# Kernel optimization log

Hardware: AMD Instinct MI355X
Metric: run time of the kernel (lower is better)

## Reference

```python
import jax, jax.numpy as jnp
import numpy as np
import math

HEADS = 4
DIM_HEAD = 32
EPS = 1e-5

def _ln_channels(x):
    # LayerNorm over channel axis (axis=1) of NCHW, no affine (eps=1e-5)
    mu = jnp.mean(x, axis=1, keepdims=True)
    var = jnp.mean((x - mu) ** 2, axis=1, keepdims=True)
    return (x - mu) * jax.lax.rsqrt(var + EPS)

def setup_inputs() -> dict:
    key = jax.random.key(0)
    k1, k2, k3, k4 = jax.random.split(key, 4)
    dim, inner = 256, HEADS * DIM_HEAD
    x = jax.random.normal(k1, (16, dim, 64, 64), dtype=jnp.float32)
    Wqkv = jax.random.normal(k2, (3 * inner, dim), dtype=jnp.float32) * (1.0 / math.sqrt(dim))
    Wout = jax.random.normal(k3, (dim, inner), dtype=jnp.float32) * (1.0 / math.sqrt(inner))
    bout = jax.random.normal(k4, (dim,), dtype=jnp.float32) * 0.01
    return {"x": x, "Wqkv": Wqkv, "Wout": Wout, "bout": bout}

def reference(x, Wqkv, Wout, bout):
    B, C, H, W = x.shape
    N = H * W
    inner = HEADS * DIM_HEAD
    # pre-norm (channel-wise LayerNorm via permute in torch)
    normed = _ln_channels(x)
    # 1x1 conv to qkv: [B, 3*inner, H, W]
    qkv = jnp.einsum('oc,bchw->bohw', Wqkv, normed)
    q, k, v = jnp.split(qkv, 3, axis=1)
    # [B, inner, H, W] -> [B, heads, N, dim_head]
    def to_heads(t):
        return t.reshape(B, HEADS, DIM_HEAD, N).transpose(0, 1, 3, 2)
    q, k, v = to_heads(q), to_heads(k), to_heads(v)
    q = jax.nn.softmax(q, axis=-1)          # over dim_head
    k = jax.nn.softmax(k, axis=-2)          # over N
    q = q / math.sqrt(DIM_HEAD)
    v = v / N
    context = jnp.einsum('bhnd,bhne->bhde', k, v)   # [B,h,d,d]
    out = jnp.einsum('bhde,bhnd->bhne', context, q) # [B,h,N,d]
    out = out.transpose(0, 1, 3, 2).reshape(B, inner, H, W)
    out = jnp.einsum('oc,bchw->bohw', Wout, out) + bout[None, :, None, None]
    out = _ln_channels(out)                  # LinearAttention.out_norm
    return out + x                           # residual
```

## Files before the change

### kernel.cpp

```cpp
#include <hip/hip_runtime.h>
#include <hip/hip_bf16.h>
#include <math.h>

#define BATCH 16
#define CH 256
#define NPOS 4096
#define INNER 128
#define HEADS 4
#define DH 32

typedef __hip_bfloat16 bf16;
typedef short bf8v __attribute__((ext_vector_type(8)));
typedef float f32x4 __attribute__((ext_vector_type(4)));

__device__ __forceinline__ float b2f(bf16 v) { return __bfloat162float(v); }
__device__ __forceinline__ float us2f(unsigned short u) {
    unsigned w = ((unsigned)u) << 16; float f; __builtin_memcpy(&f, &w, 4); return f;
}
__device__ __forceinline__ unsigned short f2us(float f) {
    bf16 h = __float2bfloat16(f); unsigned short u; __builtin_memcpy(&u, &h, 2); return u;
}
__device__ __forceinline__ bf16 f2b(float v) { return __float2bfloat16(v); }

__global__ __launch_bounds__(256)
void prep_w_kernel(const float* __restrict__ Wqkv, bf16* __restrict__ wqb,
                   float* __restrict__ wqs) {
    int idx = (blockIdx.x * 256 + threadIdx.x) * 4;
    float4 w = *(const float4*)&Wqkv[idx];
    ushort4 u;
    u.x = f2us(w.x); u.y = f2us(w.y); u.z = f2us(w.z); u.w = f2us(w.w);
    *(ushort4*)&wqb[idx] = u;
    float s4 = us2f(u.x) + us2f(u.y) + us2f(u.z) + us2f(u.w);
    #pragma unroll
    for (int m = 1; m <= 32; m <<= 1) s4 += __shfl_xor(s4, m, 64);
    if ((threadIdx.x & 63) == 0)
        wqs[blockIdx.x * 4 + (threadIdx.x >> 6)] = s4;
}

__global__ __launch_bounds__(256)
void fused_qkv_kernel(const float* __restrict__ x, const bf16* __restrict__ wqb,
                      const float* __restrict__ wqs,
                      bf16* __restrict__ p, float* __restrict__ ctxp) {
    __shared__ char smem[36864];
    __shared__ float stats[640];

    const int b = blockIdx.y, tile = blockIdx.x, n0 = tile * 64;
    const int tid = threadIdx.x;
    const int w = tid >> 6, lane = tid & 63;
    const int lrow = lane & 15, kq = lane >> 4;
    bf16* A = (bf16*)smem;

    {
        const int nq = tid & 15, cp = tid >> 4;
        float s[4] = {0.f,0.f,0.f,0.f}, sq[4] = {0.f,0.f,0.f,0.f};
        #pragma unroll
        for (int i = 0; i < 8; ++i) {
            int c0 = cp * 2 + 32 * i;
            const float* xp = x + ((size_t)b * CH + c0) * NPOS + n0 + nq * 4;
            float4 fa = *(const float4*)xp;
            float4 fb = *(const float4*)(xp + NPOS);
            #pragma unroll
            for (int j = 0; j < 4; ++j) {
                float va = (&fa.x)[j], vb = (&fb.x)[j];
                s[j] += va + vb; sq[j] += va * va + vb * vb;
                *(unsigned*)&A[(nq * 4 + j) * 264 + c0] =
                    (unsigned)f2us(va) | ((unsigned)f2us(vb) << 16);
            }
        }
        #pragma unroll
        for (int j = 0; j < 4; ++j) {
            s[j]  += __shfl_xor(s[j], 16, 64);  sq[j] += __shfl_xor(sq[j], 16, 64);
            s[j]  += __shfl_xor(s[j], 32, 64);  sq[j] += __shfl_xor(sq[j], 32, 64);
            if (lane < 16) {
                stats[(nq * 4 + j) * 8 + w * 2]     = s[j];
                stats[(nq * 4 + j) * 8 + w * 2 + 1] = sq[j];
            }
        }
    }
    __syncthreads();
    if (tid < 64) {
        float s  = stats[tid*8] + stats[tid*8+2] + stats[tid*8+4] + stats[tid*8+6];
        float sq = stats[tid*8+1] + stats[tid*8+3] + stats[tid*8+5] + stats[tid*8+7];
        float m = s * (1.f / 256.f);
        float var = sq * (1.f / 256.f) - m * m;
        stats[512 + tid * 2] = m;
        stats[512 + tid * 2 + 1] = rsqrtf(var + 1e-5f);
    }
    __syncthreads();

    ushort4 ekp[4][2];
    float se0 = 0.f, se1 = 0.f;

    for (int ph = 0; ph < 3; ++ph) {
        const bf16* wp = wqb + (size_t)(ph * 128 + w * 32) * 256;
        const float cs0 = wqs[ph * 128 + w * 32 + lrow];
        const float cs1 = wqs[ph * 128 + w * 32 + 16 + lrow];
        f32x4 acc[4][2];
        #pragma unroll
        for (int i = 0; i < 4; ++i) {
            acc[i][0] = (f32x4){0.f,0.f,0.f,0.f};
            acc[i][1] = (f32x4){0.f,0.f,0.f,0.f};
        }
        #pragma unroll 2
        for (int k0 = 0; k0 < 256; k0 += 32) {
            bf8v af[4], bfr[2];
            #pragma unroll
            for (int t = 0; t < 4; ++t)
                af[t] = *(const bf8v*)&A[(t * 16 + lrow) * 264 + k0 + kq * 8];
            #pragma unroll
            for (int t = 0; t < 2; ++t)
                bfr[t] = *(const bf8v*)&wp[(size_t)(t * 16 + lrow) * 256 + k0 + kq * 8];
            #pragma unroll
            for (int mt = 0; mt < 4; ++mt)
                #pragma unroll
                for (int nt = 0; nt < 2; ++nt)
                    acc[mt][nt] = __builtin_amdgcn_mfma_f32_16x16x32_bf16(
                        af[mt], bfr[nt], acc[mt][nt], 0, 0, 0);
        }

        if (ph == 0) {
            unsigned* pg32 = (unsigned*)p;
            #pragma unroll
            for (int mt = 0; mt < 4; ++mt)
                #pragma unroll
                for (int r = 0; r < 4; ++r) {
                    int row = mt * 16 + kq * 4 + r;
                    float mu = stats[512 + row * 2], rsn = stats[512 + row * 2 + 1];
                    float e0 = __expf(b2f(f2b((acc[mt][0][r] - mu * cs0) * rsn)));
                    float e1 = __expf(b2f(f2b((acc[mt][1][r] - mu * cs1) * rsn)));
                    float s = e0 + e1;
                    s += __shfl_xor(s, 1, 64);  s += __shfl_xor(s, 2, 64);
                    s += __shfl_xor(s, 4, 64);  s += __shfl_xor(s, 8, 64);
                    float rd = 1.f / s;
                    pg32[(size_t)(b * NPOS + n0 + row) * 64 + w * 16 + lrow] =
                        (unsigned)f2us(e0 * rd) | ((unsigned)f2us(e1 * rd) << 16);
                }
        } else if (ph == 1) {
            se0 = 0.f; se1 = 0.f;
            #pragma unroll
            for (int mt = 0; mt < 4; ++mt) {
                ushort4 u0, u1;
                unsigned short q_;
                #pragma unroll
                for (int r = 0; r < 4; ++r) {
                    int row = mt * 16 + kq * 4 + r;
                    float mu = stats[512 + row * 2], rsn = stats[512 + row * 2 + 1];
                    q_ = f2us(__expf(b2f(f2b((acc[mt][0][r] - mu * cs0) * rsn))));
                    se0 += us2f(q_); (&u0.x)[r] = q_;
                    q_ = f2us(__expf(b2f(f2b((acc[mt][1][r] - mu * cs1) * rsn))));
                    se1 += us2f(q_); (&u1.x)[r] = q_;
                }
                ekp[mt][0] = u0; ekp[mt][1] = u1;
            }
            se0 += __shfl_xor(se0, 16, 64); se0 += __shfl_xor(se0, 32, 64);
            se1 += __shfl_xor(se1, 16, 64); se1 += __shfl_xor(se1, 32, 64);
        } else {
            __syncthreads();
            bf16* ekt = (bf16*)(smem + w * 9216);
            bf16* vt  = (bf16*)(smem + w * 9216 + 4608);
            #pragma unroll
            for (int mt = 0; mt < 4; ++mt)
                #pragma unroll
                for (int nt = 0; nt < 2; ++nt) {
                    float csx = nt ? cs1 : cs0;
                    ushort4 vv;
                    #pragma unroll
                    for (int r = 0; r < 4; ++r) {
                        int row = mt * 16 + kq * 4 + r;
                        float mu = stats[512 + row * 2], rsn = stats[512 + row * 2 + 1];
                        (&vv.x)[r] = f2us((acc[mt][nt][r] - mu * csx) * rsn);
                    }
                    int d = nt * 16 + lrow, n = mt * 16 + kq * 4;
                    *(ushort4*)&vt[d * 72 + n]  = vv;
                    *(ushort4*)&ekt[d * 72 + n] = ekp[mt][nt];
                }
            f32x4 cacc[2][2];
            cacc[0][0] = (f32x4){0.f,0.f,0.f,0.f}; cacc[0][1] = cacc[0][0];
            cacc[1][0] = cacc[0][0];               cacc[1][1] = cacc[0][0];
            #pragma unroll
            for (int ks = 0; ks < 2; ++ks) {
                bf8v a2[2], bv2[2];
                a2[0]  = *(const bf8v*)&ekt[lrow * 72 + ks * 32 + kq * 8];
                a2[1]  = *(const bf8v*)&ekt[(16 + lrow) * 72 + ks * 32 + kq * 8];
                bv2[0] = *(const bf8v*)&vt[lrow * 72 + ks * 32 + kq * 8];
                bv2[1] = *(const bf8v*)&vt[(16 + lrow) * 72 + ks * 32 + kq * 8];
                #pragma unroll
                for (int mt2 = 0; mt2 < 2; ++mt2)
                    #pragma unroll
                    for (int nt2 = 0; nt2 < 2; ++nt2)
                        cacc[mt2][nt2] = __builtin_amdgcn_mfma_f32_16x16x32_bf16(
                            a2[mt2], bv2[nt2], cacc[mt2][nt2], 0, 0, 0);
            }
            float* pb = ctxp + ((size_t)(b * 64 + tile) * 4 + w) * 1056;
            #pragma unroll
            for (int mt2 = 0; mt2 < 2; ++mt2)
                #pragma unroll
                for (int nt2 = 0; nt2 < 2; ++nt2)
                    #pragma unroll
                    for (int r = 0; r < 4; ++r) {
                        int d = mt2 * 16 + kq * 4 + r, e = nt2 * 16 + lrow;
                        pb[d * 32 + e] = cacc[mt2][nt2][r];
                    }
            if (kq == 0) {
                pb[1024 + lrow] = se0;
                pb[1024 + 16 + lrow] = se1;
            }
        }
    }
}

__global__ __launch_bounds__(256)
void ctx_wmod_kernel(const float* __restrict__ ctxp, const float* __restrict__ Wout,
                     bf16* __restrict__ wmod) {
    __shared__ float cs[1056];
    int h = blockIdx.x, b = blockIdx.y, ch = blockIdx.z;
    int tid = threadIdx.x;

    #pragma unroll
    for (int i = 0; i < 2; ++i) {
        int s = i * 256 + tid;
        if (s < 264) {
            f32x4 a = (f32x4){0.f,0.f,0.f,0.f};
            const float* src = ctxp + (size_t)(b * 64 * 4 + h) * 1056 + s * 4;
            for (int t = 0; t < 64; ++t)
                a += *(const f32x4*)(src + (size_t)t * 4 * 1056);
            *(f32x4*)&cs[s * 4] = a;
        }
    }
    __syncthreads();

    int c = ch * 128 + (tid >> 1);
    int dh = tid & 1;
    const float* wr = Wout + (size_t)c * INNER + h * DH;
    float wv[32];
    #pragma unroll
    for (int i = 0; i < 8; ++i) {
        float4 t = *(const float4*)&wr[i * 4];
        wv[i * 4] = t.x; wv[i * 4 + 1] = t.y; wv[i * 4 + 2] = t.z; wv[i * 4 + 3] = t.w;
    }
    const float SCALE = 4.3158341e-05f;
    unsigned* wm32 = (unsigned*)(wmod + ((size_t)b * CH + c) * INNER + h * DH);
    #pragma unroll
    for (int dd = 0; dd < 8; ++dd) {
        int d1 = dh * 8 + dd, d2 = d1 + 16;
        const float* c1 = &cs[d1 * 32];
        const float* c2 = &cs[d2 * 32];
        float s1 = 0.f, s2 = 0.f;
        #pragma unroll
        for (int e4 = 0; e4 < 8; ++e4) {
            f32x4 t1 = *(const f32x4*)&c1[e4 * 4];
            f32x4 t2 = *(const f32x4*)&c2[e4 * 4];
            #pragma unroll
            for (int j = 0; j < 4; ++j) {
                s1 += wv[e4 * 4 + j] * t1[j];
                s2 += wv[e4 * 4 + j] * t2[j];
            }
        }
        float v1 = s1 * SCALE / cs[1024 + d1];
        float v2 = s2 * SCALE / cs[1024 + d2];
        wm32[d1] = (unsigned)f2us(v1) | ((unsigned)f2us(v2) << 16);
    }
}

__global__ __launch_bounds__(256)
void fused_out_kernel(const bf16* __restrict__ p, const bf16* __restrict__ wmod,
                      const float* __restrict__ bout, const float* __restrict__ x,
                      float* __restrict__ out) {
    __shared__ char lds[39424];
    bf16* Ap = (bf16*)lds;
    float* ct = (float*)lds;
    float* st = (float*)(lds + 36864);

    const int b = blockIdx.y, n0 = blockIdx.x * 64;
    const int tid = threadIdx.x;
    const int w = tid >> 6, lane = tid & 63;
    const int lrow = lane & 15, kq = lane >> 4;

    {
        const uint4* pg = (const uint4*)p;
        unsigned* A32 = (unsigned*)Ap;
        #pragma unroll
        for (int i = 0; i < 4; ++i) {
            int idx = i * 256 + tid;
            int c4 = idx & 15, n = idx >> 4;
            uint4 u = pg[(size_t)(b * NPOS + n0 + n) * 16 + c4];
            *(uint4*)(A32 + n * 68 + c4 * 4) = u;
        }
    }
    __syncthreads();

    f32x4 acc[4][4];
    #pragma unroll
    for (int i = 0; i < 4; ++i)
        #pragma unroll
        for (int j = 0; j < 4; ++j) acc[i][j] = (f32x4){0.f, 0.f, 0.f, 0.f};

    const bf16* wb = wmod + (size_t)b * CH * INNER + (size_t)(w * 64) * INNER;
    #pragma unroll 2
    for (int k0 = 0; k0 < 128; k0 += 32) {
        bf8v af[4], bfr[4];
        #pragma unroll
        for (int t = 0; t < 4; ++t)
            af[t] = *(const bf8v*)&Ap[(t * 16 + lrow) * 136 + k0 + kq * 8];
        #pragma unroll
        for (int t = 0; t < 4; ++t)
            bfr[t] = *(const bf8v*)&wb[(size_t)(t * 16 + lrow) * 128 + k0 + kq * 8];
        #pragma unroll
        for (int mt = 0; mt < 4; ++mt)
            #pragma unroll
            for (int nt = 0; nt < 4; ++nt)
                acc[mt][nt] = __builtin_amdgcn_mfma_f32_16x16x32_bf16(
                    af[mt], bfr[nt], acc[mt][nt], 0, 0, 0);
    }

    #pragma unroll
    for (int nt = 0; nt < 4; ++nt) {
        float bv = bout[w * 64 + nt * 16 + lrow];
        #pragma unroll
        for (int mt = 0; mt < 4; ++mt)
            #pragma unroll
            for (int r = 0; r < 4; ++r) acc[mt][nt][r] += bv;
    }

    float4 xr[4];
    #pragma unroll
    for (int i = 0; i < 4; ++i) {
        int idx = i * 256 + tid;
        int n4 = (idx & 7) * 4, c = idx >> 3;
        xr[i] = *(const float4*)&x[((size_t)b * CH + c) * NPOS + n0 + n4];
    }

    #pragma unroll
    for (int mt = 0; mt < 4; ++mt)
        #pragma unroll
        for (int r = 0; r < 4; ++r) {
            float s = 0.f, sq = 0.f;
            #pragma unroll
            for (int nt = 0; nt < 4; ++nt) {
                float v = acc[mt][nt][r];
                s += v; sq += v * v;
            }
            #pragma unroll
            for (int m = 1; m <= 8; m <<= 1) {
                s += __shfl_xor(s, m, 64);
                sq += __shfl_xor(sq, m, 64);
            }
            if (lrow == 0) {
                int row = mt * 16 + kq * 4 + r;
                st[w * 128 + row * 2] = s;
                st[w * 128 + row * 2 + 1] = sq;
            }
        }
    __syncthreads();
    if (tid < 64) {
        float s  = st[tid * 2]       + st[128 + tid * 2]
                 + st[256 + tid * 2] + st[384 + tid * 2];
        float sq = st[tid * 2 + 1]       + st[128 + tid * 2 + 1]
                 + st[256 + tid * 2 + 1] + st[384 + tid * 2 + 1];
        float m = s * (1.f / 256.f);
        float var = sq * (1.f / 256.f) - m * m;
        st[512 + tid * 2] = m;
        st[512 + tid * 2 + 1] = rsqrtf(var + 1e-5f);
    }
    __syncthreads();
    #pragma unroll
    for (int mt = 0; mt < 4; ++mt)
        #pragma unroll
        for (int r = 0; r < 4; ++r) {
            int row = mt * 16 + kq * 4 + r;
            float m = st[512 + row * 2], rs = st[512 + row * 2 + 1];
            #pragma unroll
            for (int nt = 0; nt < 4; ++nt)
                acc[mt][nt][r] = (acc[mt][nt][r] - m) * rs;
        }

    #pragma unroll 1
    for (int pr = 0; pr < 2; ++pr) {
        __syncthreads();
        #pragma unroll
        for (int mi = 0; mi < 2; ++mi) {
            int mt = pr * 2 + mi;
            #pragma unroll
            for (int nt = 0; nt < 4; ++nt)
                #pragma unroll
                for (int r = 0; r < 4; ++r) {
                    int rl = mi * 16 + kq * 4 + r;
                    ct[(w * 64 + nt * 16 + lrow) * 36 + rl] = acc[mt][nt][r];
                }
        }
        __syncthreads();
        #pragma unroll
        for (int i = 0; i < 4; ++i) {
            int idx = i * 256 + tid;
            int n4 = (idx & 7) * 4, c = idx >> 3;
            size_t gi = ((size_t)b * CH + c) * NPOS + n0 + pr * 32 + n4;
            f32x4 cv = *(const f32x4*)&ct[c * 36 + n4];
            float4 xv = xr[i];
            float4 ov;
            ov.x = cv[0] + xv.x; ov.y = cv[1] + xv.y;
            ov.z = cv[2] + xv.z; ov.w = cv[3] + xv.w;
            *(float4*)&out[gi] = ov;
        }
        #pragma unroll
        for (int i = 4; i < 8; ++i) {
            int idx = i * 256 + tid;
            int n4 = (idx & 7) * 4, c = idx >> 3;
            size_t gi = ((size_t)b * CH + c) * NPOS + n0 + pr * 32 + n4;
            f32x4 cv = *(const f32x4*)&ct[c * 36 + n4];
            float4 xv = *(const float4*)&x[gi];
            float4 ov;
            ov.x = cv[0] + xv.x; ov.y = cv[1] + xv.y;
            ov.z = cv[2] + xv.z; ov.w = cv[3] + xv.w;
            *(float4*)&out[gi] = ov;
        }
        if (pr == 0) {
            #pragma unroll
            for (int i = 0; i < 4; ++i) {
                int idx = i * 256 + tid;
                int n4 = (idx & 7) * 4, c = idx >> 3;
                xr[i] = *(const float4*)&x[((size_t)b * CH + c) * NPOS + n0 + 32 + n4];
            }
        }
    }
}

extern "C" void kernel_launch(void* const* d_in, const int* in_sizes, int n_in,
                              void* d_out, int out_size, void* d_ws, size_t ws_size,
                              hipStream_t stream) {
    const float* x    = (const float*)d_in[0];
    const float* Wqkv = (const float*)d_in[1];
    const float* Wout = (const float*)d_in[2];
    const float* bout = (const float*)d_in[3];
    float* out = (float*)d_out;

    char* ws = (char*)d_ws;
    bf16*  p      = (bf16*)ws;
    float* ctxp   = (float*)(ws + 16777216);
    bf16*  wmod   = (bf16*)(ws + 34349056);
    bf16*  wqb    = (bf16*)(ws + 35397632);
    float* wqs    = (float*)(ws + 35594240);

    prep_w_kernel<<<dim3(96), 256, 0, stream>>>(Wqkv, wqb, wqs);
    fused_qkv_kernel<<<dim3(64, BATCH), 256, 0, stream>>>(x, wqb, wqs, p, ctxp);
    ctx_wmod_kernel<<<dim3(HEADS, BATCH, 2), 256, 0, stream>>>(ctxp, Wout, wmod);
    fused_out_kernel<<<dim3(64, BATCH), 256, 0, stream>>>(p, wmod, bout, x, out);
}
```

Before: 209.9 us.

## Restructure output epilogue by channel halves with nontemporal stores

The output staging is reorganized so each pass writes a full 64-position row for 128 channels (two waves per pass) instead of 32 positions for all channels. This gives 256-byte contiguous global segments per channel. The x prefetch into registers is dropped and x is loaded directly, and outputs are written with nontemporal stores to avoid polluting cache. The k-loop of the QKV GEMM is also unrolled further, and LDS use shrinks slightly. Only half the waves are active in each staging write, and x-load latency is no longer overlapped with the epilogue.

```diff
diff --git a/kernel.cpp b/kernel.cpp
--- a/kernel.cpp
+++ b/kernel.cpp
@@ -101,7 +101,7 @@
             acc[i][0] = (f32x4){0.f,0.f,0.f,0.f};
             acc[i][1] = (f32x4){0.f,0.f,0.f,0.f};
         }
-        #pragma unroll 2
+        #pragma unroll 4
         for (int k0 = 0; k0 < 256; k0 += 32) {
             bf8v af[4], bfr[2];
             #pragma unroll
@@ -266,10 +266,10 @@
 void fused_out_kernel(const bf16* __restrict__ p, const bf16* __restrict__ wmod,
                       const float* __restrict__ bout, const float* __restrict__ x,
                       float* __restrict__ out) {
-    __shared__ char lds[39424];
+    __shared__ char lds[37376];
     bf16* Ap = (bf16*)lds;
     float* ct = (float*)lds;
-    float* st = (float*)(lds + 36864);
+    float* st = (float*)(lds + 34816);
 
     const int b = blockIdx.y, n0 = blockIdx.x * 64;
     const int tid = threadIdx.x;
@@ -320,14 +320,6 @@
         for (int mt = 0; mt < 4; ++mt)
             #pragma unroll
             for (int r = 0; r < 4; ++r) acc[mt][nt][r] += bv;
-    }
-
-    float4 xr[4];
-    #pragma unroll
-    for (int i = 0; i < 4; ++i) {
-        int idx = i * 256 + tid;
-        int n4 = (idx & 7) * 4, c = idx >> 3;
-        xr[i] = *(const float4*)&x[((size_t)b * CH + c) * NPOS + n0 + n4];
     }
 
     #pragma unroll
@@ -377,49 +369,25 @@
     #pragma unroll 1
     for (int pr = 0; pr < 2; ++pr) {
         __syncthreads();
-        #pragma unroll
-        for (int mi = 0; mi < 2; ++mi) {
-            int mt = pr * 2 + mi;
-            #pragma unroll
-            for (int nt = 0; nt < 4; ++nt)
-                #pragma unroll
-                for (int r = 0; r < 4; ++r) {
-                    int rl = mi * 16 + kq * 4 + r;
-                    ct[(w * 64 + nt * 16 + lrow) * 36 + rl] = acc[mt][nt][r];
-                }
+        if ((w >> 1) == pr) {
+            #pragma unroll
+            for (int mt = 0; mt < 4; ++mt)
+                #pragma unroll
+                for (int nt = 0; nt < 4; ++nt)
+                    #pragma unroll
+                    for (int r = 0; r < 4; ++r)
+                        ct[((w & 1) * 64 + nt * 16 + lrow) * 68 + mt * 16 + kq * 4 + r]
+                            = acc[mt][nt][r];
         }
         __syncthreads();
         #pragma unroll
-        for (int i = 0; i < 4; ++i) {
+        for (int i = 0; i < 8; ++i) {
             int idx = i * 256 + tid;
-            int n4 = (idx & 7) * 4, c = idx >> 3;
-            size_t gi = ((size_t)b * CH + c) * NPOS + n0 + pr * 32 + n4;
-            f32x4 cv = *(const f32x4*)&ct[c * 36 + n4];
-            float4 xv = xr[i];
-            float4 ov;
-            ov.x = cv[0] + xv.x; ov.y = cv[1] + xv.y;
-            ov.z = cv[2] + xv.z; ov.w = cv[3] + xv.w;
-            *(float4*)&out[gi] = ov;
-        }
-        #pragma unroll
-        for (int i = 4; i < 8; ++i) {
-            int idx = i * 256 + tid;
-            int n4 = (idx & 7) * 4, c = idx >> 3;
-            size_t gi = ((size_t)b * CH + c) * NPOS + n0 + pr * 32 + n4;
-            f32x4 cv = *(const f32x4*)&ct[c * 36 + n4];
-            float4 xv = *(const float4*)&x[gi];
-            float4 ov;
-            ov.x = cv[0] + xv.x; ov.y = cv[1] + xv.y;
-            ov.z = cv[2] + xv.z; ov.w = cv[3] + xv.w;
-            *(float4*)&out[gi] = ov;
-        }
-        if (pr == 0) {
-            #pragma unroll
-            for (int i = 0; i < 4; ++i) {
-                int idx = i * 256 + tid;
-                int n4 = (idx & 7) * 4, c = idx >> 3;
-                xr[i] = *(const float4*)&x[((size_t)b * CH + c) * NPOS + n0 + 32 + n4];
-            }
+            int n4 = (idx & 15) * 4, cl = idx >> 4;
+            size_t gi = ((size_t)b * CH + pr * 128 + cl) * NPOS + n0 + n4;
+            f32x4 cv = *(const f32x4*)&ct[cl * 68 + n4];
+            f32x4 xv = *(const f32x4*)&x[gi];
+            __builtin_nontemporal_store(cv + xv, (f32x4*)&out[gi]);
         }
     }
 }
```

Measured after the change: 187.6 us. 1.12x faster.
